# Kernel optimization log

Measured on AMD Instinct MI355X. Metric: run time of the kernel, lower is better.

The kernel has to match this reference:

```python
import jax, jax.numpy as jnp
import numpy as np

N_NODES = 100000
N_EDGES = 1600000
IN_FEAT = 48
OUT_FEAT = 48


def setup_inputs() -> dict:
    key = jax.random.key(0)
    k_h, k_src, k_dst, k_tw, k_tb, k_pw, k_pb = jax.random.split(key, 7)
    lim = 1.0 / np.sqrt(IN_FEAT)  # nn.Linear default init range
    return {
        "h": jax.random.normal(k_h, (N_NODES, IN_FEAT), dtype=jnp.float32),
        "theta_w": jax.random.uniform(k_tw, (OUT_FEAT, IN_FEAT), jnp.float32, -lim, lim),
        "theta_b": jax.random.uniform(k_tb, (OUT_FEAT,), jnp.float32, -lim, lim),
        "phi_w": jax.random.uniform(k_pw, (OUT_FEAT, IN_FEAT), jnp.float32, -lim, lim),
        "phi_b": jax.random.uniform(k_pb, (OUT_FEAT,), jnp.float32, -lim, lim),
        "src": jax.random.randint(k_src, (N_EDGES,), 0, N_NODES, dtype=jnp.int64),
        "dst": jax.random.randint(k_dst, (N_EDGES,), 0, N_NODES, dtype=jnp.int64),
    }


def reference(h, theta_w, theta_b, phi_w, phi_b, src, dst):
    # phi is applied to source node features only -> compute per-node then gather (cheaper, same math)
    phi_all = h @ phi_w.T + phi_b                      # [N, Dout]
    diff = h[dst] - h[src]                             # [E, Din]  (edges.dst['x'] - edges.src['x'])
    e = diff @ theta_w.T + theta_b + phi_all[src]      # [E, Dout] per-edge message
    # scatter-max over incoming edges per destination node
    out = jax.ops.segment_max(e, dst, num_segments=N_NODES)  # [N, Dout]
    # nodes with no in-edges: DGL yields 0, segment_max yields -inf -> replace
    out = jnp.where(jnp.isneginf(out), 0.0, out)
    return out
```

## Files before the change

### kernel.cpp

```cpp
#include <hip/hip_runtime.h>
#include <math.h>

#define DIN 48
#define DOUT 48
#define NPB 128
#define NB_MAX 800
#define BIN_BLOCKS 512
#define EPB_MAX 3136
#define SCAP 2432
#define INIT_KEY 0x007FFFFFu

typedef short s16x8 __attribute__((ext_vector_type(8)));
typedef float f32x4v __attribute__((ext_vector_type(4)));

__device__ __forceinline__ float funkey(unsigned k) {
  unsigned b = (k & 0x80000000u) ? (k & 0x7FFFFFFFu) : ~k;
  return __uint_as_float(b);
}
__device__ __forceinline__ unsigned bfkey(unsigned u16) {
  unsigned b = u16 << 16;
  return (b & 0x80000000u) ? ~b : (b | 0x80000000u);
}
__device__ __forceinline__ unsigned short f2bf(float f) {
  unsigned u = __float_as_uint(f);
  return (unsigned short)((u + 0x7fffu + ((u >> 16) & 1u)) >> 16);
}

__global__ __launch_bounds__(256) void prep(
    const float* __restrict__ tw, const float* __restrict__ tb,
    const float* __restrict__ pw, const float* __restrict__ pb,
    unsigned short* __restrict__ wcs, float* __restrict__ bias) {
  int i = blockIdx.x * 256 + threadIdx.x;
  if (i < 6144) {
    int j = i & 7;
    int fragpos = i >> 3;
    int lane = fragpos & 63;
    int frag = fragpos >> 6;
    int kstep = frag & 1;
    int ntile = frag >> 1;
    int feat = ntile * 16 + (lane & 15);
    int k = kstep * 32 + (lane >> 4) * 8 + j;
    float v = 0.f;
    if (k < DIN) {
      v = (feat < DOUT) ? tw[feat * DIN + k]
                        : pw[(feat - DOUT) * DIN + k] - tw[(feat - DOUT) * DIN + k];
    }
    wcs[i] = f2bf(v);
  } else if (i < 6144 + 96) {
    int f = i - 6144;
    bias[f] = (f < DOUT) ? tb[f] : pb[f - DOUT];
  }
}

__device__ __forceinline__ void transform_body(
    int bid, const float* __restrict__ h, const unsigned short* __restrict__ wcs,
    const float* __restrict__ bias, float* __restrict__ A,
    unsigned short* __restrict__ Bh, int n_nodes) {
  int t = threadIdx.x;
  int wave = t >> 6, lane = t & 63;
  int quad = lane >> 4, nl = lane & 15;
  int vb = bid * 64 + wave * 16;
  int vload = vb + nl;

  s16x8 a0 = {0, 0, 0, 0, 0, 0, 0, 0};
  s16x8 a1 = {0, 0, 0, 0, 0, 0, 0, 0};
  if (vload < n_nodes) {
    const float* hp = h + (size_t)vload * DIN;
    float4 x = *reinterpret_cast<const float4*>(hp + quad * 8);
    float4 y = *reinterpret_cast<const float4*>(hp + quad * 8 + 4);
    a0[0] = (short)f2bf(x.x); a0[1] = (short)f2bf(x.y);
    a0[2] = (short)f2bf(x.z); a0[3] = (short)f2bf(x.w);
    a0[4] = (short)f2bf(y.x); a0[5] = (short)f2bf(y.y);
    a0[6] = (short)f2bf(y.z); a0[7] = (short)f2bf(y.w);
    if (quad < 2) {
      float4 z = *reinterpret_cast<const float4*>(hp + 32 + quad * 8);
      float4 u = *reinterpret_cast<const float4*>(hp + 32 + quad * 8 + 4);
      a1[0] = (short)f2bf(z.x); a1[1] = (short)f2bf(z.y);
      a1[2] = (short)f2bf(z.z); a1[3] = (short)f2bf(z.w);
      a1[4] = (short)f2bf(u.x); a1[5] = (short)f2bf(u.y);
      a1[6] = (short)f2bf(u.z); a1[7] = (short)f2bf(u.w);
    }
  }

  const s16x8* wf = reinterpret_cast<const s16x8*>(wcs);
  f32x4v acc[6];
#pragma unroll
  for (int nt = 0; nt < 6; ++nt) {
    float bv = bias[nt * 16 + nl];
    acc[nt] = (f32x4v){bv, bv, bv, bv};
  }
#pragma unroll
  for (int nt = 0; nt < 6; ++nt) {
    s16x8 b0 = wf[(nt * 2 + 0) * 64 + lane];
    s16x8 b1 = wf[(nt * 2 + 1) * 64 + lane];
    acc[nt] = __builtin_amdgcn_mfma_f32_16x16x32_bf16(a0, b0, acc[nt], 0, 0, 0);
    acc[nt] = __builtin_amdgcn_mfma_f32_16x16x32_bf16(a1, b1, acc[nt], 0, 0, 0);
  }

#pragma unroll
  for (int reg = 0; reg < 4; ++reg) {
    int v = vb + quad * 4 + reg;
    if (v < n_nodes) {
#pragma unroll
      for (int nt = 0; nt < 3; ++nt)
        A[(size_t)v * DOUT + nt * 16 + nl] = acc[nt][reg];
#pragma unroll
      for (int nt = 3; nt < 6; ++nt)
        Bh[(size_t)v * DOUT + (nt - 3) * 16 + nl] = f2bf(acc[nt][reg]);
    }
  }
}

__device__ __forceinline__ void bin_body(
    int r, unsigned* __restrict__ shmem,
    const int* __restrict__ src, const int* __restrict__ dst,
    unsigned* __restrict__ ebuf, unsigned* __restrict__ soffsT,
    int n_edges, int nbucket, int epb) {
  unsigned* rec = shmem;
  unsigned short* rbkt = (unsigned short*)(rec + EPB_MAX);
  unsigned* cnt = (unsigned*)(rbkt + EPB_MAX);
  unsigned* part = cnt + NB_MAX;
  int t = threadIdx.x;
  for (int b = t; b < nbucket; b += 256) cnt[b] = 0;
  __syncthreads();

  int start = r * epb;
  int nrec = n_edges - start;
  if (nrec > epb) nrec = epb;
  if (nrec < 0) nrec = 0;

  for (int k = t; k < nrec; k += 256) {
    int s = src[start + k], d = dst[start + k];
    int b = d >> 7;
    rec[k] = ((unsigned)(d & (NPB - 1)) << 17) | (unsigned)s;
    rbkt[k] = (unsigned short)b;
    atomicAdd(&cnt[b], 1u);
  }
  __syncthreads();

  int per = (nbucket + 255) / 256;
  unsigned local[8];
  unsigned s = 0;
#pragma unroll 4
  for (int i = 0; i < per; ++i) {
    int idx = t * per + i;
    local[i] = (idx < nbucket) ? cnt[idx] : 0u;
    s += local[i];
  }
  part[t] = s;
  __syncthreads();
  for (int off = 1; off < 256; off <<= 1) {
    unsigned v = (t >= off) ? part[t - off] : 0u;
    __syncthreads();
    part[t] += v;
    __syncthreads();
  }
  unsigned run = part[t] - s;
#pragma unroll 4
  for (int i = 0; i < per; ++i) {
    int idx = t * per + i;
    if (idx < nbucket) {
      cnt[idx] = run;
      soffsT[(size_t)idx * BIN_BLOCKS + r] = run;
      run += local[i];
    }
  }
  if (t == 0) soffsT[(size_t)nbucket * BIN_BLOCKS + r] = (unsigned)nrec;
  __syncthreads();

  for (int k = t; k < nrec; k += 256) {
    unsigned p = atomicAdd(&cnt[rbkt[k]], 1u);
    ebuf[(size_t)r * epb + p] = rec[k];
  }
}

__global__ __launch_bounds__(256) void nt_bin(
    const float* __restrict__ h, const unsigned short* __restrict__ wcs,
    const float* __restrict__ bias, float* __restrict__ A,
    unsigned short* __restrict__ Bh, const int* __restrict__ src,
    const int* __restrict__ dst, unsigned* __restrict__ ebuf,
    unsigned* __restrict__ soffsT, int n_nodes, int n_edges, int nbucket,
    int epb, int nt_blocks) {
  __shared__ unsigned shmem[EPB_MAX + EPB_MAX / 2 + NB_MAX + 256];
  int bid = blockIdx.x;
  if (bid < nt_blocks)
    transform_body(bid, h, wcs, bias, A, Bh, n_nodes);
  else
    bin_body(bid - nt_blocks, shmem, src, dst, ebuf, soffsT, n_edges, nbucket, epb);
}

#define BM_THREADS 512
#define BM_GROUPS 42
#define PFD 8
__global__ __launch_bounds__(BM_THREADS) void bucket_max(
    const unsigned* __restrict__ ebuf, const unsigned* __restrict__ soffsT,
    const unsigned short* __restrict__ Bh, float* __restrict__ out,
    int n_nodes, int epb) {
  __shared__ unsigned keys[NPB * DOUT];
  __shared__ unsigned srecs[SCAP];
  __shared__ unsigned part[BM_THREADS];
  __shared__ unsigned total_sh;
  int t = threadIdx.x;
  int bkt = blockIdx.x;

#pragma unroll
  for (int i = t; i < NPB * DOUT; i += BM_THREADS) keys[i] = INIT_KEY;

  unsigned a = soffsT[(size_t)bkt * BIN_BLOCKS + t];
  unsigned b = soffsT[(size_t)(bkt + 1) * BIN_BLOCKS + t];
  unsigned len = b - a;
  part[t] = len;
  __syncthreads();
  for (int off = 1; off < BM_THREADS; off <<= 1) {
    unsigned v = (t >= off) ? part[t - off] : 0u;
    __syncthreads();
    part[t] += v;
    __syncthreads();
  }
  unsigned base = part[t] - len;
  if (t == BM_THREADS - 1) total_sh = part[t];
  {
    const unsigned* ep = ebuf + (size_t)t * epb + a;
    for (unsigned i = 0; i < len; ++i) {
      unsigned p = base + i;
      if (p < (unsigned)SCAP) srecs[p] = ep[i];
    }
  }
  __syncthreads();
  int total = (int)total_sh;
  if (total > SCAP) total = SCAP;

  int g = t / 12;
  int c = t % 12;
  if (g < BM_GROUPS) {
    int lo = g * total / BM_GROUPS;
    int hi = (g + 1) * total / BM_GROUPS;
    for (int j = lo; j < hi; j += PFD) {
      int n = hi - j;
      if (n > PFD) n = PFD;
      unsigned rr[PFD];
      uint2 bb[PFD];
#pragma unroll
      for (int p = 0; p < PFD; ++p)
        if (p < n) rr[p] = srecs[j + p];
#pragma unroll
      for (int p = 0; p < PFD; ++p)
        if (p < n)
          bb[p] = *reinterpret_cast<const uint2*>(
              Bh + (size_t)(rr[p] & 0x1FFFF) * DOUT + c * 4);
#pragma unroll
      for (int p = 0; p < PFD; ++p) {
        if (p < n) {
          unsigned* kp = &keys[(rr[p] >> 17) * DOUT + c * 4];
          atomicMax(&kp[0], bfkey(bb[p].x & 0xffffu));
          atomicMax(&kp[1], bfkey(bb[p].x >> 16));
          atomicMax(&kp[2], bfkey(bb[p].y & 0xffffu));
          atomicMax(&kp[3], bfkey(bb[p].y >> 16));
        }
      }
    }
  }
  __syncthreads();

  int node0 = bkt * NPB;
  for (int i = t; i < NPB * (DOUT / 4); i += BM_THREADS) {
    int n = i / (DOUT / 4), cc = i % (DOUT / 4);
    int v = node0 + n;
    if (v < n_nodes) {
      unsigned* kp = &keys[n * DOUT + 4 * cc];
      unsigned k0 = kp[0], k1 = kp[1], k2 = kp[2], k3 = kp[3];
      float4* op = reinterpret_cast<float4*>(out + (size_t)v * DOUT + 4 * cc);
      float4 aa = *op;
      float4 r;
      r.x = (k0 == INIT_KEY) ? 0.f : aa.x + funkey(k0);
      r.y = (k1 == INIT_KEY) ? 0.f : aa.y + funkey(k1);
      r.z = (k2 == INIT_KEY) ? 0.f : aa.z + funkey(k2);
      r.w = (k3 == INIT_KEY) ? 0.f : aa.w + funkey(k3);
      *op = r;
    }
  }
}

extern "C" void kernel_launch(void* const* d_in, const int* in_sizes, int n_in,
                              void* d_out, int out_size, void* d_ws, size_t ws_size,
                              hipStream_t stream) {
  const float* h  = (const float*)d_in[0];
  const float* tw = (const float*)d_in[1];
  const float* tb = (const float*)d_in[2];
  const float* pw = (const float*)d_in[3];
  const float* pb = (const float*)d_in[4];
  const int* src  = (const int*)d_in[5];
  const int* dst  = (const int*)d_in[6];
  int n_nodes = in_sizes[0] / DIN;
  int n_edges = in_sizes[5];
  int nbucket = (n_nodes + NPB - 1) / NPB;
  int epb = (n_edges + BIN_BLOCKS - 1) / BIN_BLOCKS;

  unsigned short* Bh  = (unsigned short*)d_ws;
  unsigned* ebuf      = (unsigned*)(Bh + (size_t)n_nodes * DOUT);
  unsigned* soffsT    = ebuf + (size_t)BIN_BLOCKS * epb;
  unsigned short* wcs = (unsigned short*)(soffsT + (size_t)(nbucket + 1) * BIN_BLOCKS);
  float* bias         = (float*)(wcs + 6144);
  float* A            = (float*)d_out;

  int nt_blocks = (n_nodes + 63) / 64;

  prep<<<25, 256, 0, stream>>>(tw, tb, pw, pb, wcs, bias);
  nt_bin<<<nt_blocks + BIN_BLOCKS, 256, 0, stream>>>(
      h, wcs, bias, A, Bh, src, dst, ebuf, soffsT, n_nodes, n_edges, nbucket,
      epb, nt_blocks);
  bucket_max<<<nbucket, BM_THREADS, 0, stream>>>(ebuf, soffsT, Bh, A, n_nodes, epb);
}
```

Measured before the change: 163.2 us.

## Fuse weight prep into transform and halve nodes per destination bucket

Drops the separate prep kernel: each transform wave now loads the fp32 theta/phi weights directly, converts them to bf16 fragments and forms phi minus theta in registers, which saves one launch and a dependent kernel boundary. It also halves the nodes per bucket from 128 to 64, doubling the bucket count. That gives the bucket_max stage twice as many smaller blocks, with smaller shared-memory staging. In exchange every transform block redoes the weight conversion, and binning gains more buckets and more prefix-scan work per block; there is also a leftover redundant weight load.

```diff
diff --git a/kernel.cpp b/kernel.cpp
--- a/kernel.cpp
+++ b/kernel.cpp
@@ -3,11 +3,11 @@
 
 #define DIN 48
 #define DOUT 48
-#define NPB 128
-#define NB_MAX 800
+#define NPB 64
+#define NB_MAX 1600
 #define BIN_BLOCKS 512
 #define EPB_MAX 3136
-#define SCAP 2432
+#define SCAP 1344
 #define INIT_KEY 0x007FFFFFu
 
 typedef short s16x8 __attribute__((ext_vector_type(8)));
@@ -26,35 +26,33 @@
   return (unsigned short)((u + 0x7fffu + ((u >> 16) & 1u)) >> 16);
 }
 
-__global__ __launch_bounds__(256) void prep(
-    const float* __restrict__ tw, const float* __restrict__ tb,
-    const float* __restrict__ pw, const float* __restrict__ pb,
-    unsigned short* __restrict__ wcs, float* __restrict__ bias) {
-  int i = blockIdx.x * 256 + threadIdx.x;
-  if (i < 6144) {
-    int j = i & 7;
-    int fragpos = i >> 3;
-    int lane = fragpos & 63;
-    int frag = fragpos >> 6;
-    int kstep = frag & 1;
-    int ntile = frag >> 1;
-    int feat = ntile * 16 + (lane & 15);
-    int k = kstep * 32 + (lane >> 4) * 8 + j;
-    float v = 0.f;
-    if (k < DIN) {
-      v = (feat < DOUT) ? tw[feat * DIN + k]
-                        : pw[(feat - DOUT) * DIN + k] - tw[(feat - DOUT) * DIN + k];
-    }
-    wcs[i] = f2bf(v);
-  } else if (i < 6144 + 96) {
-    int f = i - 6144;
-    bias[f] = (f < DOUT) ? tb[f] : pb[f - DOUT];
-  }
+__device__ __forceinline__ s16x8 ldfrag_t(const float* __restrict__ w, int row) {
+  const float4* p = reinterpret_cast<const float4*>(w + row * DIN);
+  float4 x = p[0], y = p[1];
+  s16x8 r;
+  r[0] = (short)f2bf(x.x); r[1] = (short)f2bf(x.y);
+  r[2] = (short)f2bf(x.z); r[3] = (short)f2bf(x.w);
+  r[4] = (short)f2bf(y.x); r[5] = (short)f2bf(y.y);
+  r[6] = (short)f2bf(y.z); r[7] = (short)f2bf(y.w);
+  return r;
+}
+__device__ __forceinline__ s16x8 ldfrag_d(const float* __restrict__ tw,
+                                          const float* __restrict__ pw, int row) {
+  const float4* a = reinterpret_cast<const float4*>(tw + row * DIN);
+  const float4* b = reinterpret_cast<const float4*>(pw + row * DIN);
+  float4 xa = a[0], ya = a[1], xb = b[0], yb = b[1];
+  s16x8 r;
+  r[0] = (short)f2bf(xb.x - xa.x); r[1] = (short)f2bf(xb.y - xa.y);
+  r[2] = (short)f2bf(xb.z - xa.z); r[3] = (short)f2bf(xb.w - xa.w);
+  r[4] = (short)f2bf(yb.x - ya.x); r[5] = (short)f2bf(yb.y - ya.y);
+  r[6] = (short)f2bf(yb.z - ya.z); r[7] = (short)f2bf(yb.w - ya.w);
+  return r;
 }
 
 __device__ __forceinline__ void transform_body(
-    int bid, const float* __restrict__ h, const unsigned short* __restrict__ wcs,
-    const float* __restrict__ bias, float* __restrict__ A,
+    int bid, const float* __restrict__ h, const float* __restrict__ tw,
+    const float* __restrict__ tb, const float* __restrict__ pw,
+    const float* __restrict__ pb, float* __restrict__ A,
     unsigned short* __restrict__ Bh, int n_nodes) {
   int t = threadIdx.x;
   int wave = t >> 6, lane = t & 63;
@@ -82,17 +80,30 @@
     }
   }
 
-  const s16x8* wf = reinterpret_cast<const s16x8*>(wcs);
   f32x4v acc[6];
 #pragma unroll
   for (int nt = 0; nt < 6; ++nt) {
-    float bv = bias[nt * 16 + nl];
+    int feat = nt * 16 + nl;
+    float bv = (nt < 3) ? tb[feat] : pb[feat - DOUT];
     acc[nt] = (f32x4v){bv, bv, bv, bv};
   }
+  s16x8 zfrag = {0, 0, 0, 0, 0, 0, 0, 0};
 #pragma unroll
   for (int nt = 0; nt < 6; ++nt) {
-    s16x8 b0 = wf[(nt * 2 + 0) * 64 + lane];
-    s16x8 b1 = wf[(nt * 2 + 1) * 64 + lane];
+    int feat = nt * 16 + nl;
+    s16x8 b0, b1;
+    if (nt < 3) {
+      b0 = ldfrag_t(tw, feat);
+      b0 = ldfrag_t(tw + quad * 8 - quad * 8, feat);
+    }
+    if (nt < 3) {
+      b0 = ldfrag_t(tw + quad * 8, feat);
+      b1 = (quad < 2) ? ldfrag_t(tw + 32 + quad * 8, feat) : zfrag;
+    } else {
+      b0 = ldfrag_d(tw + quad * 8, pw + quad * 8, feat - DOUT);
+      b1 = (quad < 2) ? ldfrag_d(tw + 32 + quad * 8, pw + 32 + quad * 8, feat - DOUT)
+                      : zfrag;
+    }
     acc[nt] = __builtin_amdgcn_mfma_f32_16x16x32_bf16(a0, b0, acc[nt], 0, 0, 0);
     acc[nt] = __builtin_amdgcn_mfma_f32_16x16x32_bf16(a1, b1, acc[nt], 0, 0, 0);
   }
@@ -131,7 +142,7 @@
 
   for (int k = t; k < nrec; k += 256) {
     int s = src[start + k], d = dst[start + k];
-    int b = d >> 7;
+    int b = d >> 6;
     rec[k] = ((unsigned)(d & (NPB - 1)) << 17) | (unsigned)s;
     rbkt[k] = (unsigned short)b;
     atomicAdd(&cnt[b], 1u);
@@ -141,7 +152,7 @@
   int per = (nbucket + 255) / 256;
   unsigned local[8];
   unsigned s = 0;
-#pragma unroll 4
+#pragma unroll 7
   for (int i = 0; i < per; ++i) {
     int idx = t * per + i;
     local[i] = (idx < nbucket) ? cnt[idx] : 0u;
@@ -156,7 +167,7 @@
     __syncthreads();
   }
   unsigned run = part[t] - s;
-#pragma unroll 4
+#pragma unroll 7
   for (int i = 0; i < per; ++i) {
     int idx = t * per + i;
     if (idx < nbucket) {
@@ -175,8 +186,9 @@
 }
 
 __global__ __launch_bounds__(256) void nt_bin(
-    const float* __restrict__ h, const unsigned short* __restrict__ wcs,
-    const float* __restrict__ bias, float* __restrict__ A,
+    const float* __restrict__ h, const float* __restrict__ tw,
+    const float* __restrict__ tb, const float* __restrict__ pw,
+    const float* __restrict__ pb, float* __restrict__ A,
     unsigned short* __restrict__ Bh, const int* __restrict__ src,
     const int* __restrict__ dst, unsigned* __restrict__ ebuf,
     unsigned* __restrict__ soffsT, int n_nodes, int n_edges, int nbucket,
@@ -184,7 +196,7 @@
   __shared__ unsigned shmem[EPB_MAX + EPB_MAX / 2 + NB_MAX + 256];
   int bid = blockIdx.x;
   if (bid < nt_blocks)
-    transform_body(bid, h, wcs, bias, A, Bh, n_nodes);
+    transform_body(bid, h, tw, tb, pw, pb, A, Bh, n_nodes);
   else
     bin_body(bid - nt_blocks, shmem, src, dst, ebuf, soffsT, n_edges, nbucket, epb);
 }
@@ -296,18 +308,15 @@
   int nbucket = (n_nodes + NPB - 1) / NPB;
   int epb = (n_edges + BIN_BLOCKS - 1) / BIN_BLOCKS;
 
-  unsigned short* Bh  = (unsigned short*)d_ws;
-  unsigned* ebuf      = (unsigned*)(Bh + (size_t)n_nodes * DOUT);
-  unsigned* soffsT    = ebuf + (size_t)BIN_BLOCKS * epb;
-  unsigned short* wcs = (unsigned short*)(soffsT + (size_t)(nbucket + 1) * BIN_BLOCKS);
-  float* bias         = (float*)(wcs + 6144);
-  float* A            = (float*)d_out;
+  unsigned short* Bh = (unsigned short*)d_ws;
+  unsigned* ebuf     = (unsigned*)(Bh + (size_t)n_nodes * DOUT);
+  unsigned* soffsT   = ebuf + (size_t)BIN_BLOCKS * epb;
+  float* A           = (float*)d_out;
 
   int nt_blocks = (n_nodes + 63) / 64;
 
-  prep<<<25, 256, 0, stream>>>(tw, tb, pw, pb, wcs, bias);
   nt_bin<<<nt_blocks + BIN_BLOCKS, 256, 0, stream>>>(
-      h, wcs, bias, A, Bh, src, dst, ebuf, soffsT, n_nodes, n_edges, nbucket,
-      epb, nt_blocks);
+      h, tw, tb, pw, pb, A, Bh, src, dst, ebuf, soffsT, n_nodes, n_edges,
+      nbucket, epb, nt_blocks);
   bucket_max<<<nbucket, BM_THREADS, 0, stream>>>(ebuf, soffsT, Bh, A, n_nodes, epb);
 }
```

After: 166.5 us. About the same (+2.0%).
